# Optimization experiments

Hardware: AMD Instinct MI355X
Metric: run time of the kernel (lower is better)

## Reference

```python
import jax, jax.numpy as jnp
import numpy as np

B, N, K = 64, 512, 32   # batch, node_num, top_k
D = 64                  # dim == embed_dim == input_dim == out_channels
EPS = 1e-5
NEG_SLOPE = 0.2         # LeakyReLU slope in GraphLayer.message
NEG_INF = -1e9


def setup_inputs() -> dict:
    key = jax.random.key(0)
    ks = jax.random.split(key, 20)
    rn = lambda k, shp, s=1.0: jax.random.normal(k, shp, jnp.float32) * s
    return {
        "data": rn(ks[0], (B, N, D)),
        "org_edge_index": jax.random.randint(ks[1], (2, 1024), 0, N),
        "emb_table": rn(ks[2], (N, D)),                 # nn.Embedding(node_num, dim)
        "lin_W": rn(ks[3], (D, D), 1.0 / np.sqrt(D)),   # GraphLayer.lin (no bias)
        "att_i": rn(ks[4], (D,), 0.1),
        "att_j": rn(ks[5], (D,), 0.1),
        "att_em_i": rn(ks[6], (D,), 0.1),
        "att_em_j": rn(ks[7], (D,), 0.1),
        "gnn_bias": rn(ks[8], (D,), 0.1),
        "bn1_gamma": 1.0 + rn(ks[9], (D,), 0.1),
        "bn1_beta": rn(ks[10], (D,), 0.1),
        "bn1_mean": rn(ks[11], (D,), 0.1),
        "bn1_var": 0.5 + jax.random.uniform(ks[12], (D,), jnp.float32),
        "bno_gamma": 1.0 + rn(ks[13], (D,), 0.1),
        "bno_beta": rn(ks[14], (D,), 0.1),
        "bno_mean": rn(ks[15], (D,), 0.1),
        "bno_var": 0.5 + jax.random.uniform(ks[16], (D,), jnp.float32),
        "out_W": rn(ks[17], (1, D), 1.0 / np.sqrt(D)),  # OutLayer single Linear(dim,1)
        "out_b": rn(ks[18], (1,), 0.1),
    }


def _gdn_forward(data, emb_table, lin_W, att_i, att_j, att_em_i, att_em_j, gnn_bias,
                 bn1_gamma, bn1_beta, bn1_mean, bn1_var,
                 bno_gamma, bno_beta, bno_mean, bno_var, out_W, out_b):
    Bn, Nn, Fin = data.shape
    x = data.reshape(-1, Fin)                               # [B*N, Fin]

    # --- dynamic graph: cosine-sim topk on detached embedding ---
    w = jax.lax.stop_gradient(emb_table)                    # weights_arr = emb.detach()
    nrm = jnp.linalg.norm(w, axis=-1)
    cos = (w @ w.T) / (nrm[:, None] * nrm[None, :])         # [N, N]
    topk_idx = jax.lax.top_k(cos, K)[1]                     # [N, K]
    src0 = topk_idx.reshape(-1)                             # j (sources)
    dst0 = jnp.repeat(jnp.arange(Nn), K)                    # i (targets)
    valid0 = src0 != dst0                                   # remove_self_loops
    offs = (jnp.arange(Bn) * Nn)[:, None]
    src = (src0[None, :] + offs).reshape(-1)                # [B*N*K]
    dst = (dst0[None, :] + offs).reshape(-1)
    valid = jnp.tile(valid0, Bn)
    loops = jnp.arange(Bn * Nn)                             # add_self_loops
    src = jnp.concatenate([src, loops])
    dst = jnp.concatenate([dst, loops])
    valid = jnp.concatenate([valid, jnp.ones(Bn * Nn, bool)])

    # --- GraphLayer (heads=1, concat=False) ---
    xl = x @ lin_W.T                                        # [B*N, D]
    src_l = src % Nn                                        # embedding tiled over batch
    dst_l = dst % Nn
    a = (xl[dst] @ att_i + emb_table[dst_l] @ att_em_i
         + xl[src] @ att_j + emb_table[src_l] @ att_em_j)   # [E]
    a = jnp.where(a >= 0, a, NEG_SLOPE * a)                 # leaky_relu
    a = jnp.where(valid, a, NEG_INF)
    seg = Bn * Nn
    amax = jax.ops.segment_max(a, dst, num_segments=seg)    # stable softmax per target
    ex = jnp.where(valid, jnp.exp(a - amax[dst]), 0.0)
    denom = jax.ops.segment_sum(ex, dst, num_segments=seg)
    alpha = ex / denom[dst]                                 # [E]
    agg = jax.ops.segment_sum(xl[src] * alpha[:, None], dst, num_segments=seg) + gnn_bias

    # --- GNNLayer BN (eval) + relu ---
    h = (agg - bn1_mean) / jnp.sqrt(bn1_var + EPS) * bn1_gamma + bn1_beta
    h = jax.nn.relu(h).reshape(Bn, Nn, -1)

    # --- mul by node embedding, BN over channels (eval), relu, dropout(eval)=id ---
    h = h * emb_table[None]
    h = (h - bno_mean) / jnp.sqrt(bno_var + EPS) * bno_gamma + bno_beta
    h = jax.nn.relu(h)

    # --- OutLayer: single Linear(dim, 1) ---
    out = h @ out_W.T + out_b                               # [B, N, 1]
    return out.reshape(-1, Nn)                              # [B, N]


def reference(data, org_edge_index, emb_table, lin_W, att_i, att_j, att_em_i, att_em_j,
              gnn_bias, bn1_gamma, bn1_beta, bn1_mean, bn1_var,
              bno_gamma, bno_beta, bno_mean, bno_var, out_W, out_b):
    # org_edge_index is accepted but unused by GDN.forward (dynamic graph replaces it)
    del org_edge_index
    return _gdn_forward(data, emb_table, lin_W, att_i, att_j, att_em_i, att_em_j, gnn_bias,
                        bn1_gamma, bn1_beta, bn1_mean, bn1_var,
                        bno_gamma, bno_beta, bno_mean, bno_var, out_W, out_b)
```

## Files before the change

kernel.cpp:

```cpp
#include <hip/hip_runtime.h>
#include <hip/hip_bf16.h>
#include <math.h>

#define BB 64
#define NN 512
#define KK 32
#define DD 64
#define BN (BB*NN)
#define EPSC 1e-5f
#define NEG_SLOPE 0.2f
#define NEG_INF_A (-1e9f)

typedef unsigned long long ull;


__global__ void k0_prep(const float* __restrict__ emb,
                        const float* __restrict__ att_em_i,
                        const float* __restrict__ att_em_j,
                        const float* __restrict__ gnn_bias,
                        const float* __restrict__ g1, const float* __restrict__ b1,
                        const float* __restrict__ m1, const float* __restrict__ v1,
                        const float* __restrict__ go, const float* __restrict__ bo,
                        const float* __restrict__ mo, const float* __restrict__ vo,
                        float* __restrict__ en, float* __restrict__ ei,
                        float* __restrict__ ej, float* __restrict__ epi) {
    const int t = threadIdx.x;
    const int lane = t & 63;
    const int wave = t >> 6;
    const int i = blockIdx.x * 4 + wave;
    const float x = emb[i*DD + lane];
    float ss = x*x;
    float e1 = x * att_em_i[lane];
    float e2 = x * att_em_j[lane];
    #pragma unroll
    for (int m = 32; m > 0; m >>= 1) {
        ss += __shfl_xor(ss, m);
        e1 += __shfl_xor(e1, m);
        e2 += __shfl_xor(e2, m);
    }
    en[i*DD + lane] = x * rsqrtf(ss);
    if (lane == 0) { ei[i] = e1; ej[i] = e2; }
    if (blockIdx.x == 0 && t < DD) {
        float s1 = g1[t] / sqrtf(v1[t] + EPSC);
        float B1 = (gnn_bias[t] - m1[t]) * s1 + b1[t];
        float so = go[t] / sqrtf(vo[t] + EPSC);
        float Bo = bo[t] - mo[t] * so;
        epi[t] = s1; epi[DD + t] = B1; epi[2*DD + t] = so; epi[3*DD + t] = Bo;
    }
}

__global__ void kA_cos(const float* __restrict__ en, ull* __restrict__ keys) {
    __shared__ float4 As[256];
    const int t = threadIdx.x;
    const int lane = t & 63;
    const int wave = t >> 6;
    const int bi = blockIdx.x >> 3;
    const int c0 = (blockIdx.x & 7) * 64;
    const float4* en4 = (const float4*)en;

    float4 Wr[16];
    #pragma unroll
    for (int q = 0; q < 16; ++q) Wr[q] = en4[(c0 + lane)*16 + q];

    As[t] = en4[bi*256 + t];
    __syncthreads();

    #pragma unroll
    for (int r = 0; r < 4; ++r) {
        const int jr = wave*4 + r;
        float acc = 0.f;
        #pragma unroll
        for (int q = 0; q < 16; ++q) {
            const float4 a = As[jr*16 + q];
            const float4 w = Wr[q];
            acc += a.x*w.x + a.y*w.y + a.z*w.z + a.w*w.w;
        }
        const int row = bi*16 + jr;
        const int col = c0 + lane;
        unsigned int u = __float_as_uint(acc);
        u = (u & 0x80000000u) ? ~u : (u | 0x80000000u);
        keys[row*NN + col] = ((ull)u << 16) | (ull)(NN - 1 - col);
    }
}

__global__ void kB_rank(const ull* __restrict__ keys, int* __restrict__ topk) {
    __shared__ ull ks[NN];
    const int i = blockIdx.x;
    const int t = threadIdx.x;
    ks[t] = keys[i*NN + t];
    __syncthreads();
    const ull mykey = ks[t];
    int rank = 0;
    #pragma unroll 16
    for (int kk = 0; kk < NN; ++kk) rank += (ks[kk] > mykey) ? 1 : 0;
    if (rank < KK) topk[i*KK + rank] = t;
}

__global__ void k2_lin(const float* __restrict__ data,
                       const float* __restrict__ linW,
                       const float* __restrict__ att_i, const float* __restrict__ att_j,
                       const float* __restrict__ ei, const float* __restrict__ ej,
                       float* __restrict__ xl, float* __restrict__ si,
                       float* __restrict__ sj) {
    __shared__ float4 xs[256];
    const int t = threadIdx.x;
    const int lane = t & 63;
    const int wave = t >> 6;

    float4 Wr[16];
    const float4* W4 = (const float4*)linW;
    #pragma unroll
    for (int q = 0; q < 16; ++q) Wr[q] = W4[lane*16 + q];

    xs[t] = ((const float4*)data)[blockIdx.x*256 + t];
    __syncthreads();

    const int r0 = wave * 4;
    float acc0 = 0.f, acc1 = 0.f, acc2 = 0.f, acc3 = 0.f;
    #pragma unroll
    for (int q = 0; q < 16; ++q) {
        const float4 w = Wr[q];
        const float4 x0 = xs[(r0+0)*16 + q];
        const float4 x1 = xs[(r0+1)*16 + q];
        const float4 x2 = xs[(r0+2)*16 + q];
        const float4 x3 = xs[(r0+3)*16 + q];
        acc0 += x0.x*w.x + x0.y*w.y + x0.z*w.z + x0.w*w.w;
        acc1 += x1.x*w.x + x1.y*w.y + x1.z*w.z + x1.w*w.w;
        acc2 += x2.x*w.x + x2.y*w.y + x2.z*w.z + x2.w*w.w;
        acc3 += x3.x*w.x + x3.y*w.y + x3.z*w.z + x3.w*w.w;
    }

    const int vbase = blockIdx.x*16 + r0;
    xl[(vbase+0)*DD + lane] = acc0;
    xl[(vbase+1)*DD + lane] = acc1;
    xl[(vbase+2)*DD + lane] = acc2;
    xl[(vbase+3)*DD + lane] = acc3;

    const float ai = att_i[lane];
    const float aj = att_j[lane];
    float accs[4] = {acc0, acc1, acc2, acc3};
    #pragma unroll
    for (int r = 0; r < 4; ++r) {
        float pi = accs[r] * ai;
        float pj = accs[r] * aj;
        #pragma unroll
        for (int m = 32; m > 0; m >>= 1) {
            pi += __shfl_xor(pi, m);
            pj += __shfl_xor(pj, m);
        }
        if (lane == 0) {
            const int v = vbase + r;
            si[v] = pi + ei[v & (NN-1)];
            sj[v] = pj + ej[v & (NN-1)];
        }
    }
}

__global__ void k3_agg(const float* __restrict__ xl, const float* __restrict__ si,
                       const float* __restrict__ sj, const int* __restrict__ topk,
                       const float* __restrict__ emb,
                       const float* __restrict__ epi,
                       const float* __restrict__ outW, const float* __restrict__ outb,
                       float* __restrict__ out) {
    const int t = threadIdx.x;
    const int lane = t & 63;
    const int wave = t >> 6;
    const int tgt = blockIdx.x * 4 + wave;
    const int b = tgt >> 9;
    const int i = tgt & (NN - 1);

    const bool isedge = (lane <= KK);
    int tk = i;
    bool valid = true;
    if (lane < KK) { tk = topk[i*KK + lane]; valid = (tk != i); }
    const int srcg = b * NN + tk;

    float a;
    if (isedge) {
        a = si[tgt] + sj[srcg];
        a = (a >= 0.f) ? a : NEG_SLOPE * a;
        if (!valid) a = NEG_INF_A;
    } else {
        a = -3.0e38f;
    }

    float amax = a;
    #pragma unroll
    for (int m = 32; m > 0; m >>= 1) amax = fmaxf(amax, __shfl_xor(amax, m));

    float ex = (isedge && valid) ? __expf(a - amax) : 0.f;
    float denom = ex;
    #pragma unroll
    for (int m = 32; m > 0; m >>= 1) denom += __shfl_xor(denom, m);
    const float alpha = ex * __builtin_amdgcn_rcpf(denom);

    const int c4 = lane & 15;
    const int e4 = lane >> 4;
    const float4* xl4 = (const float4*)xl;
    float4 acc = make_float4(0.f, 0.f, 0.f, 0.f);
    #pragma unroll
    for (int m = 0; m < 8; ++m) {
        const int kk = 4*m + e4;
        const float al = __shfl(alpha, kk);
        const int   sg = __shfl(srcg, kk);
        const float4 xv = xl4[sg*16 + c4];
        acc.x += al*xv.x; acc.y += al*xv.y; acc.z += al*xv.z; acc.w += al*xv.w;
    }
    {
        const float al = __shfl(alpha, KK);
        const int   sg = __shfl(srcg, KK);
        if (e4 == 0) {
            const float4 xv = xl4[sg*16 + c4];
            acc.x += al*xv.x; acc.y += al*xv.y; acc.z += al*xv.z; acc.w += al*xv.w;
        }
    }
    #pragma unroll
    for (int m = 16; m <= 32; m <<= 1) {
        acc.x += __shfl_xor(acc.x, m);
        acc.y += __shfl_xor(acc.y, m);
        acc.z += __shfl_xor(acc.z, m);
        acc.w += __shfl_xor(acc.w, m);
    }

    const float4* epi4 = (const float4*)epi;
    const float4 s1 = epi4[c4];
    const float4 B1 = epi4[16 + c4];
    const float4 so = epi4[32 + c4];
    const float4 Bo = epi4[48 + c4];
    const float4 em = ((const float4*)emb)[i*16 + c4];
    const float4 w4 = ((const float4*)outW)[c4];
    float4 h;
    h.x = fmaxf(acc.x*s1.x + B1.x, 0.f) * em.x;
    h.y = fmaxf(acc.y*s1.y + B1.y, 0.f) * em.y;
    h.z = fmaxf(acc.z*s1.z + B1.z, 0.f) * em.z;
    h.w = fmaxf(acc.w*s1.w + B1.w, 0.f) * em.w;
    h.x = fmaxf(h.x*so.x + Bo.x, 0.f);
    h.y = fmaxf(h.y*so.y + Bo.y, 0.f);
    h.z = fmaxf(h.z*so.z + Bo.z, 0.f);
    h.w = fmaxf(h.w*so.w + Bo.w, 0.f);
    float p = h.x*w4.x + h.y*w4.y + h.z*w4.z + h.w*w4.w;
    p += __shfl_xor(p, 1);
    p += __shfl_xor(p, 2);
    p += __shfl_xor(p, 4);
    p += __shfl_xor(p, 8);
    if (lane == 0) out[tgt] = p + outb[0];
}

extern "C" void kernel_launch(void* const* d_in, const int* in_sizes, int n_in,
                              void* d_out, int out_size, void* d_ws, size_t ws_size,
                              hipStream_t stream) {
    (void)in_sizes; (void)n_in; (void)out_size; (void)ws_size;
    const float* data   = (const float*)d_in[0];
    const float* emb    = (const float*)d_in[2];
    const float* linW   = (const float*)d_in[3];
    const float* att_i  = (const float*)d_in[4];
    const float* att_j  = (const float*)d_in[5];
    const float* attemi = (const float*)d_in[6];
    const float* attemj = (const float*)d_in[7];
    const float* gbias  = (const float*)d_in[8];
    const float* g1     = (const float*)d_in[9];
    const float* b1     = (const float*)d_in[10];
    const float* m1     = (const float*)d_in[11];
    const float* v1     = (const float*)d_in[12];
    const float* go     = (const float*)d_in[13];
    const float* bo     = (const float*)d_in[14];
    const float* mo     = (const float*)d_in[15];
    const float* vo     = (const float*)d_in[16];
    const float* outW   = (const float*)d_in[17];
    const float* outb   = (const float*)d_in[18];
    float* out = (float*)d_out;

    char* ws = (char*)d_ws;
    float* ei   = (float*)(ws + 0);
    float* ej   = (float*)(ws + 4096);
    float* epi  = (float*)(ws + 8192);
    int*   topk = (int*)  (ws + 16384);
    float* si   = (float*)(ws + 81920);
    float* sj   = (float*)(ws + 212992);
    float* en   = (float*)(ws + 344064);
    float* xl   = (float*)(ws + 475136);
    ull*   keys = (ull*)  (ws + 475136);

    k0_prep<<<NN/4, 256, 0, stream>>>(emb, attemi, attemj, gbias,
                                      g1, b1, m1, v1, go, bo, mo, vo,
                                      en, ei, ej, epi);
    kA_cos<<<256, 256, 0, stream>>>(en, keys);
    kB_rank<<<NN, NN, 0, stream>>>(keys, topk);
    k2_lin<<<BN/16, 256, 0, stream>>>(data, linW, att_i, att_j, ei, ej,
                                      xl, si, sj);
    k3_agg<<<BN/4, 256, 0, stream>>>(xl, si, sj, topk, emb, epi,
                                     outW, outb, out);
}
```

Measured before the change: 153.4 us.

## Fuse prep kernel into cosine and rank kernels; stage weights via LDS

```diff
diff --git a/kernel.cpp b/kernel.cpp
--- a/kernel.cpp
+++ b/kernel.cpp
@@ -14,55 +14,45 @@
 typedef unsigned long long ull;
 
 
-__global__ void k0_prep(const float* __restrict__ emb,
-                        const float* __restrict__ att_em_i,
-                        const float* __restrict__ att_em_j,
-                        const float* __restrict__ gnn_bias,
-                        const float* __restrict__ g1, const float* __restrict__ b1,
-                        const float* __restrict__ m1, const float* __restrict__ v1,
-                        const float* __restrict__ go, const float* __restrict__ bo,
-                        const float* __restrict__ mo, const float* __restrict__ vo,
-                        float* __restrict__ en, float* __restrict__ ei,
-                        float* __restrict__ ej, float* __restrict__ epi) {
-    const int t = threadIdx.x;
-    const int lane = t & 63;
-    const int wave = t >> 6;
-    const int i = blockIdx.x * 4 + wave;
-    const float x = emb[i*DD + lane];
-    float ss = x*x;
-    float e1 = x * att_em_i[lane];
-    float e2 = x * att_em_j[lane];
-    #pragma unroll
-    for (int m = 32; m > 0; m >>= 1) {
-        ss += __shfl_xor(ss, m);
-        e1 += __shfl_xor(e1, m);
-        e2 += __shfl_xor(e2, m);
-    }
-    en[i*DD + lane] = x * rsqrtf(ss);
-    if (lane == 0) { ei[i] = e1; ej[i] = e2; }
-    if (blockIdx.x == 0 && t < DD) {
-        float s1 = g1[t] / sqrtf(v1[t] + EPSC);
-        float B1 = (gnn_bias[t] - m1[t]) * s1 + b1[t];
-        float so = go[t] / sqrtf(vo[t] + EPSC);
-        float Bo = bo[t] - mo[t] * so;
-        epi[t] = s1; epi[DD + t] = B1; epi[2*DD + t] = so; epi[3*DD + t] = Bo;
-    }
-}
-
-__global__ void kA_cos(const float* __restrict__ en, ull* __restrict__ keys) {
+__global__ void kA_cos(const float* __restrict__ emb, ull* __restrict__ keys) {
     __shared__ float4 As[256];
+    __shared__ float4 Bs[1024];
+    __shared__ float rsA[16];
     const int t = threadIdx.x;
     const int lane = t & 63;
     const int wave = t >> 6;
     const int bi = blockIdx.x >> 3;
     const int c0 = (blockIdx.x & 7) * 64;
-    const float4* en4 = (const float4*)en;
+    const float4* emb4 = (const float4*)emb;
+
+    As[t] = emb4[bi*256 + t];
+    Bs[t]       = emb4[c0*16 + t];
+    Bs[t + 256] = emb4[c0*16 + t + 256];
+    Bs[t + 512] = emb4[c0*16 + t + 512];
+    Bs[t + 768] = emb4[c0*16 + t + 768];
+    __syncthreads();
+
+    if (wave == 0) {
+        const int r = lane >> 2, qq = lane & 3;
+        float ss = 0.f;
+        #pragma unroll
+        for (int m = 0; m < 4; ++m) {
+            const float4 a = As[r*16 + qq*4 + m];
+            ss += a.x*a.x + a.y*a.y + a.z*a.z + a.w*a.w;
+        }
+        ss += __shfl_xor(ss, 1);
+        ss += __shfl_xor(ss, 2);
+        if (qq == 0) rsA[r] = rsqrtf(ss);
+    }
 
     float4 Wr[16];
-    #pragma unroll
-    for (int q = 0; q < 16; ++q) Wr[q] = en4[(c0 + lane)*16 + q];
-
-    As[t] = en4[bi*256 + t];
+    float ssW = 0.f;
+    #pragma unroll
+    for (int q = 0; q < 16; ++q) {
+        Wr[q] = Bs[lane*16 + q];
+        ssW += Wr[q].x*Wr[q].x + Wr[q].y*Wr[q].y + Wr[q].z*Wr[q].z + Wr[q].w*Wr[q].w;
+    }
+    const float rsW = rsqrtf(ssW);
     __syncthreads();
 
     #pragma unroll
@@ -75,19 +65,51 @@
             const float4 w = Wr[q];
             acc += a.x*w.x + a.y*w.y + a.z*w.z + a.w*w.w;
         }
+        const float c = acc * rsA[jr] * rsW;
         const int row = bi*16 + jr;
         const int col = c0 + lane;
-        unsigned int u = __float_as_uint(acc);
+        unsigned int u = __float_as_uint(c);
         u = (u & 0x80000000u) ? ~u : (u | 0x80000000u);
         keys[row*NN + col] = ((ull)u << 16) | (ull)(NN - 1 - col);
     }
 }
 
-__global__ void kB_rank(const ull* __restrict__ keys, int* __restrict__ topk) {
+__global__ void kB_rank(const ull* __restrict__ keys,
+                        const float* __restrict__ emb,
+                        const float* __restrict__ att_em_i,
+                        const float* __restrict__ att_em_j,
+                        const float* __restrict__ gnn_bias,
+                        const float* __restrict__ g1, const float* __restrict__ b1,
+                        const float* __restrict__ m1, const float* __restrict__ v1,
+                        const float* __restrict__ go, const float* __restrict__ bo,
+                        const float* __restrict__ mo, const float* __restrict__ vo,
+                        int* __restrict__ topk,
+                        float* __restrict__ ei, float* __restrict__ ej,
+                        float* __restrict__ epi) {
     __shared__ ull ks[NN];
     const int i = blockIdx.x;
     const int t = threadIdx.x;
     ks[t] = keys[i*NN + t];
+
+    if (t < DD) {
+        const float e = emb[i*DD + t];
+        float e1 = e * att_em_i[t];
+        float e2 = e * att_em_j[t];
+        #pragma unroll
+        for (int m = 32; m > 0; m >>= 1) {
+            e1 += __shfl_xor(e1, m);
+            e2 += __shfl_xor(e2, m);
+        }
+        if (t == 0) { ei[i] = e1; ej[i] = e2; }
+    }
+    if (i == 0 && t >= 64 && t < 64 + DD) {
+        const int d = t - 64;
+        float s1 = g1[d] / sqrtf(v1[d] + EPSC);
+        float B1 = (gnn_bias[d] - m1[d]) * s1 + b1[d];
+        float so = go[d] / sqrtf(vo[d] + EPSC);
+        float Bo = bo[d] - mo[d] * so;
+        epi[d] = s1; epi[DD + d] = B1; epi[2*DD + d] = so; epi[3*DD + d] = Bo;
+    }
     __syncthreads();
     const ull mykey = ks[t];
     int rank = 0;
@@ -102,18 +124,23 @@
                        const float* __restrict__ ei, const float* __restrict__ ej,
                        float* __restrict__ xl, float* __restrict__ si,
                        float* __restrict__ sj) {
+    __shared__ float4 Ws[1024];
     __shared__ float4 xs[256];
     const int t = threadIdx.x;
     const int lane = t & 63;
     const int wave = t >> 6;
-
-    float4 Wr[16];
     const float4* W4 = (const float4*)linW;
-    #pragma unroll
-    for (int q = 0; q < 16; ++q) Wr[q] = W4[lane*16 + q];
-
+
+    Ws[t]       = W4[t];
+    Ws[t + 256] = W4[t + 256];
+    Ws[t + 512] = W4[t + 512];
+    Ws[t + 768] = W4[t + 768];
     xs[t] = ((const float4*)data)[blockIdx.x*256 + t];
     __syncthreads();
+
+    float4 Wr[16];
+    #pragma unroll
+    for (int q = 0; q < 16; ++q) Wr[q] = Ws[lane*16 + q];
 
     const int r0 = wave * 4;
     float acc0 = 0.f, acc1 = 0.f, acc2 = 0.f, acc3 = 0.f;
@@ -277,15 +304,13 @@
     int*   topk = (int*)  (ws + 16384);
     float* si   = (float*)(ws + 81920);
     float* sj   = (float*)(ws + 212992);
-    float* en   = (float*)(ws + 344064);
-    float* xl   = (float*)(ws + 475136);
-    ull*   keys = (ull*)  (ws + 475136);
-
-    k0_prep<<<NN/4, 256, 0, stream>>>(emb, attemi, attemj, gbias,
-                                      g1, b1, m1, v1, go, bo, mo, vo,
-                                      en, ei, ej, epi);
-    kA_cos<<<256, 256, 0, stream>>>(en, keys);
-    kB_rank<<<NN, NN, 0, stream>>>(keys, topk);
+    float* xl   = (float*)(ws + 344064);
+    ull*   keys = (ull*)  (ws + 344064);
+
+    kA_cos<<<256, 256, 0, stream>>>(emb, keys);
+    kB_rank<<<NN, NN, 0, stream>>>(keys, emb, attemi, attemj, gbias,
+                                   g1, b1, m1, v1, go, bo, mo, vo,
+                                   topk, ei, ej, epi);
     k2_lin<<<BN/16, 256, 0, stream>>>(data, linW, att_i, att_j, ei, ej,
                                       xl, si, sj);
     k3_agg<<<BN/4, 256, 0, stream>>>(xl, si, sj, topk, emb, epi,
```

Result: no change. 153.6 us (+0.1%).
